# Optimization experiments

Measured on AMD Instinct MI355X. Metric: run time of the kernel, lower is better.

The kernel has to match this reference:

```python
import jax, jax.numpy as jnp
import numpy as np

B, S, D, H = 2, 2048, 1024, 16
HD = D // H  # head_dim = 64


def setup_inputs() -> dict:
    key = jax.random.key(0)
    ks = jax.random.split(key, 7)
    s = 0.02
    return {
        "queries": jax.random.normal(ks[0], (B, S, D), jnp.float32),
        "keys": jax.random.normal(ks[1], (B, S, D), jnp.float32),
        "values": jax.random.normal(ks[2], (B, S, D), jnp.float32),
        "Wq": jax.random.normal(ks[3], (D, D), jnp.float32) * s,
        "Wk": jax.random.normal(ks[4], (D, D), jnp.float32) * s,
        "Wv": jax.random.normal(ks[5], (D, D), jnp.float32) * s,
        "Wo": jax.random.normal(ks[6], (D, D), jnp.float32) * s,
    }


def reference(queries, keys, values, Wq, Wk, Wv, Wo):
    # Projections (torch Linear: x @ W.T); split into heads -> [B, H, S, HD]
    def split_heads(x):
        b, s, _ = x.shape
        return x.reshape(b, s, H, HD).transpose(0, 2, 1, 3)

    q = split_heads(queries @ Wq.T)
    k = split_heads(keys @ Wk.T)
    v = split_heads(values @ Wv.T)

    scale = 1.0 / jnp.sqrt(jnp.asarray(HD, q.dtype))
    scores = jnp.einsum("bhqd,bhkd->bhqk", q, k) * scale  # [B,H,S,S]
    attn = jax.nn.softmax(scores, axis=-1)
    ctx = jnp.einsum("bhqk,bhkd->bhqd", attn, v)  # [B,H,S,HD]
    out = ctx.transpose(0, 2, 1, 3).reshape(queries.shape[0], -1, D)
    return out @ Wo.T
```

## Files before the change

### kernel.cpp

```cpp
#include <hip/hip_runtime.h>
#include <hip/hip_bf16.h>
#include <cstdint>


#define B_ 2
#define S_ 2048
#define D_ 1024
#define H_ 16
#define HD_ 64
#define NE_ (B_ * S_ * D_)
#define WN_ (D_ * D_)

typedef unsigned short u16;
typedef unsigned int u32;
typedef u16 __attribute__((may_alias)) u16_ma;
typedef float __attribute__((may_alias)) f32_ma;
typedef u32 v4u __attribute__((ext_vector_type(4)));
typedef v4u __attribute__((may_alias)) v4u_ma;
typedef short bf16x8 __attribute__((ext_vector_type(8)));
typedef bf16x8 __attribute__((may_alias)) bf16x8_ma;
typedef float f32x4 __attribute__((ext_vector_type(4)));

__device__ __forceinline__ float bf2f(u16 u) {
  u32 x = ((u32)u) << 16;
  return __builtin_bit_cast(float, x);
}
__device__ __forceinline__ u16 f2bf(float f) {
  __hip_bfloat16 h = __float2bfloat16(f);
  return __builtin_bit_cast(u16, h);
}
__device__ __forceinline__ u32 pk2(u32 alo, u32 ahi) {
  return (u32)f2bf(__builtin_bit_cast(float, alo)) |
         ((u32)f2bf(__builtin_bit_cast(float, ahi)) << 16);
}

__device__ __forceinline__ void gl_lds16(const u16* g, u16* l) {
  auto gp = (const __attribute__((address_space(1))) unsigned int*)(const void*)g;
  auto lp = (__attribute__((address_space(3))) unsigned int*)(void*)l;
  __builtin_amdgcn_global_load_lds(gp, lp, 16, 0, 0);
}

__device__ __forceinline__ bool detect_f32(const u16* Wg) {
  const int lane = threadIdx.x & 63;
  bool hit = false;
#pragma unroll
  for (int i = 0; i < 4; ++i) {
    v4u u = *(const v4u_ma*)(Wg + lane * 32 + i * 8);
#pragma unroll
    for (int j = 0; j < 4; ++j) {
      u32 w = u[j];
      hit |= (((w >> 7) & 0xFFu) >= 0xF0u) || (((w >> 23) & 0xFFu) >= 0xF0u);
    }
  }
  return __any(hit);
}

__global__ __launch_bounds__(256) void convert_bf16(
    const void* s0, const void* s1, const void* s2, const void* s3,
    const void* s4, const void* s5, const void* s6, u16* __restrict__ dst_in,
    u16* __restrict__ dst_w, const u16* __restrict__ Wdet) {
  const bool det = detect_f32(Wdet);
  const int y = blockIdx.y;
  const void* src;
  u16* dst;
  int n;
  if (y < 3) {
    src = (y == 0) ? s0 : ((y == 1) ? s1 : s2);
    dst = dst_in + (size_t)y * NE_;
    n = NE_;
  } else {
    src = (y == 3) ? s3 : ((y == 4) ? s4 : ((y == 5) ? s5 : s6));
    dst = dst_w + (size_t)(y - 3) * WN_;
    n = WN_;
  }
  const int i = (blockIdx.x * 256 + threadIdx.x) * 8;
  if (i >= n) return;
  v4u out;
  if (det) {
    const v4u_ma* fp = (const v4u_ma*)((const float*)src + i);
    v4u f0 = fp[0], f1 = fp[1];
    out[0] = pk2(f0[0], f0[1]);
    out[1] = pk2(f0[2], f0[3]);
    out[2] = pk2(f1[0], f1[1]);
    out[3] = pk2(f1[2], f1[3]);
  } else {
    out = *(const v4u_ma*)((const u16*)src + i);
  }
  *(v4u_ma*)(dst + i) = out;
}

template <int BN, bool OUT_DET>
__global__ __launch_bounds__(256) void proj_g(
    const u16* __restrict__ Ab, const u16* __restrict__ Wb,
    void* __restrict__ Cb, const u16* __restrict__ Wdet) {
  __shared__ u16 Al[128 * 32];
  __shared__ u16 Wl[BN * 32];

  const bool outf32 = OUT_DET ? detect_f32(Wdet) : false;

  const int tid = threadIdx.x;
  const int lane = tid & 63, wid = tid >> 6;
  const int lg = lane >> 4, li = lane & 15;
  const int wr = wid >> 1, wc = wid & 1;
  const int z = blockIdx.z;
  const u16* Ag = Ab + (size_t)z * NE_;
  const u16* Wg = Wb + (size_t)z * WN_;
  const int m0 = blockIdx.x * 128, n0 = blockIdx.y * BN;

  const int srow = wid * 16 + (lane >> 2);
  const int scol = (lane & 3) * 8;
  const u16* Asrc = Ag + (size_t)(m0 + srow) * D_ + scol;
  const u16* Wsrc = Wg + (size_t)(n0 + srow) * D_ + scol;
  u16* Adst = Al + (wid * 16) * 32;
  u16* Wdst = Wl + (wid * 16) * 32;

  constexpr int NF = BN / 32;
  f32x4 acc[4][NF];
#pragma unroll
  for (int m = 0; m < 4; ++m)
#pragma unroll
    for (int n = 0; n < NF; ++n) acc[m][n] = (f32x4){0.f, 0.f, 0.f, 0.f};

  for (int kt = 0; kt < 32; ++kt) {
    const int k0 = kt * 32;
    __syncthreads();
    gl_lds16(Asrc + k0, Adst);
    gl_lds16(Asrc + (size_t)64 * D_ + k0, Adst + 64 * 32);
    gl_lds16(Wsrc + k0, Wdst);
    if constexpr (BN == 128) gl_lds16(Wsrc + (size_t)64 * D_ + k0, Wdst + 64 * 32);
    __syncthreads();

    bf16x8 af[4], bw[NF];
#pragma unroll
    for (int m = 0; m < 4; ++m)
      af[m] = *(const bf16x8_ma*)(Al + (wr * 64 + m * 16 + li) * 32 + lg * 8);
#pragma unroll
    for (int n = 0; n < NF; ++n)
      bw[n] =
          *(const bf16x8_ma*)(Wl + (wc * (BN / 2) + n * 16 + li) * 32 + lg * 8);
#pragma unroll
    for (int m = 0; m < 4; ++m)
#pragma unroll
      for (int n = 0; n < NF; ++n)
        acc[m][n] =
            __builtin_amdgcn_mfma_f32_16x16x32_bf16(af[m], bw[n], acc[m][n], 0, 0, 0);
  }

#pragma unroll
  for (int m = 0; m < 4; ++m)
#pragma unroll
    for (int n = 0; n < NF; ++n)
#pragma unroll
      for (int r = 0; r < 4; ++r) {
        const int row = m0 + wr * 64 + m * 16 + lg * 4 + r;
        const int col = n0 + wc * (BN / 2) + n * 16 + li;
        const size_t idx = (size_t)row * D_ + col;
        const float v = acc[m][n][r];
        if (OUT_DET) {
          if (outf32)
            ((f32_ma*)Cb)[idx] = v;
          else
            ((u16_ma*)Cb)[idx] = f2bf(v);
        } else {
          ((u16_ma*)((u16*)Cb + (size_t)z * NE_))[idx] = f2bf(v);
        }
      }
}

__global__ __launch_bounds__(256) void attn_mfma2(
    const u16* __restrict__ Qg, const u16* __restrict__ Kg,
    const u16* __restrict__ Vg, u16* __restrict__ Og) {
  __shared__ u16 Kl[64 * 64];
  __shared__ u16 VTl[64 * 64];
  __shared__ u16 Pl[4][32 * 64];

  const int tid = threadIdx.x;
  const int wid = tid >> 6, lane = tid & 63;
  const int lg = lane >> 4, li = lane & 15;

  const int bid = blockIdx.x;
  const int swz = (bid & 7) * 64 + (bid >> 3);
  const int qb = swz & 15;
  const int h = (swz >> 4) & 15;
  const int b = swz >> 8;
  const size_t bbase = (size_t)b * S_ * D_;
  const int hoff = h * HD_;
  const int q0 = qb * 128 + wid * 32;

  bf16x8 aq[2][2];
#pragma unroll
  for (int qf = 0; qf < 2; ++qf) {
    const u16* qp =
        Qg + bbase + (size_t)(q0 + qf * 16 + li) * D_ + hoff + lg * 8;
    aq[qf][0] = *(const bf16x8_ma*)(qp);
    aq[qf][1] = *(const bf16x8_ma*)(qp + 32);
  }

  f32x4 o[2][4];
  float mrun[2][4], lrun[2][4];
#pragma unroll
  for (int qf = 0; qf < 2; ++qf)
#pragma unroll
    for (int t = 0; t < 4; ++t) {
      o[qf][t] = (f32x4){0.f, 0.f, 0.f, 0.f};
      mrun[qf][t] = -1e30f;
      lrun[qf][t] = 0.f;
    }

  const int krr = tid >> 3;
  const int kc8 = (tid & 7) * 8;
  const int vkr = lane;
  const int vd0 = wid * 8;

  v4u kr0, kr1, vr0, vr1;
  auto kv_load = [&](int kt) {
    const int key0 = kt * 64;
    kr0 = *(const v4u_ma*)(Kg + bbase + (size_t)(key0 + krr) * D_ + hoff + kc8);
    kr1 = *(const v4u_ma*)(Kg + bbase + (size_t)(key0 + 32 + krr) * D_ + hoff + kc8);
    vr0 = *(const v4u_ma*)(Vg + bbase + (size_t)(key0 + vkr) * D_ + hoff + vd0);
    vr1 = *(const v4u_ma*)(Vg + bbase + (size_t)(key0 + vkr) * D_ + hoff + vd0 + 32);
  };
  auto kv_write = [&]() {
    const int ksw = (krr & 7) << 4;
    *(v4u_ma*)((char*)Kl + krr * 128 + ((kc8 * 2) ^ ksw)) = kr0;
    *(v4u_ma*)((char*)Kl + (32 + krr) * 128 + ((kc8 * 2) ^ ksw)) = kr1;
    union {
      v4u v;
      u16 e[8];
    } uu;
    uu.v = vr0;
#pragma unroll
    for (int j = 0; j < 8; ++j) {
      const int d = vd0 + j;
      *(u16*)((char*)VTl + d * 128 + ((vkr * 2) ^ ((d & 7) << 4))) = uu.e[j];
    }
    uu.v = vr1;
#pragma unroll
    for (int j = 0; j < 8; ++j) {
      const int d = vd0 + 32 + j;
      *(u16*)((char*)VTl + d * 128 + ((vkr * 2) ^ ((d & 7) << 4))) = uu.e[j];
    }
  };

  kv_load(0);
  kv_write();

  for (int kt = 0; kt < S_ / 64; ++kt) {
    __syncthreads();
    if (kt < S_ / 64 - 1) kv_load(kt + 1);

    f32x4 s[2][4];
#pragma unroll
    for (int kk = 0; kk < 4; ++kk) {
      const int row = kk * 16 + li;
      const char* kb = (const char*)Kl + row * 128;
      const int sw = (row & 7) << 4;
      bf16x8 b0 = *(const bf16x8_ma*)(kb + ((lg * 16) ^ sw));
      bf16x8 b1 = *(const bf16x8_ma*)(kb + ((64 + lg * 16) ^ sw));
#pragma unroll
      for (int qf = 0; qf < 2; ++qf) {
        f32x4 z = (f32x4){0.f, 0.f, 0.f, 0.f};
        z = __builtin_amdgcn_mfma_f32_16x16x32_bf16(aq[qf][0], b0, z, 0, 0, 0);
        z = __builtin_amdgcn_mfma_f32_16x16x32_bf16(aq[qf][1], b1, z, 0, 0, 0);
        s[qf][kk] = z * 0.125f;
      }
    }

#pragma unroll
    for (int qf = 0; qf < 2; ++qf) {
      float al[4];
#pragma unroll
      for (int r = 0; r < 4; ++r) {
        float t0 =
            fmaxf(fmaxf(s[qf][0][r], s[qf][1][r]), fmaxf(s[qf][2][r], s[qf][3][r]));
#pragma unroll
        for (int off = 1; off < 16; off <<= 1) t0 = fmaxf(t0, __shfl_xor(t0, off));
        const float mn = fmaxf(mrun[qf][r], t0);
        al[r] = __expf(mrun[qf][r] - mn);
        mrun[qf][r] = mn;
      }
#pragma unroll
      for (int r = 0; r < 4; ++r) {
        s[qf][0][r] = __expf(s[qf][0][r] - mrun[qf][r]);
        s[qf][1][r] = __expf(s[qf][1][r] - mrun[qf][r]);
        s[qf][2][r] = __expf(s[qf][2][r] - mrun[qf][r]);
        s[qf][3][r] = __expf(s[qf][3][r] - mrun[qf][r]);
        float sum = s[qf][0][r] + s[qf][1][r] + s[qf][2][r] + s[qf][3][r];
#pragma unroll
        for (int off = 1; off < 16; off <<= 1) sum += __shfl_xor(sum, off);
        lrun[qf][r] = lrun[qf][r] * al[r] + sum;
      }
      const f32x4 alv = {al[0], al[1], al[2], al[3]};
#pragma unroll
      for (int t = 0; t < 4; ++t) o[qf][t] *= alv;
    }

    char* Pw = (char*)&Pl[wid][0];
#pragma unroll
    for (int qf = 0; qf < 2; ++qf)
#pragma unroll
      for (int kk = 0; kk < 4; ++kk)
#pragma unroll
        for (int r = 0; r < 4; ++r) {
          const int row = qf * 16 + lg * 4 + r;
          *(u16*)(Pw + row * 128 + (((kk * 16 + li) * 2) ^ ((row & 7) << 4))) =
              f2bf(s[qf][kk][r]);
        }
    asm volatile("s_waitcnt lgkmcnt(0)" ::: "memory");

    bf16x8 pa[2][2];
#pragma unroll
    for (int qf = 0; qf < 2; ++qf) {
      const char* pb = Pw + (qf * 16 + li) * 128;
      const int sw = (li & 7) << 4;
      pa[qf][0] = *(const bf16x8_ma*)(pb + ((lg * 16) ^ sw));
      pa[qf][1] = *(const bf16x8_ma*)(pb + ((64 + lg * 16) ^ sw));
    }

#pragma unroll
    for (int t = 0; t < 4; ++t) {
      const int row = t * 16 + li;
      const char* vb = (const char*)VTl + row * 128;
      const int sw = (row & 7) << 4;
      bf16x8 v0 = *(const bf16x8_ma*)(vb + ((lg * 16) ^ sw));
      bf16x8 v1 = *(const bf16x8_ma*)(vb + ((64 + lg * 16) ^ sw));
#pragma unroll
      for (int qf = 0; qf < 2; ++qf) {
        o[qf][t] =
            __builtin_amdgcn_mfma_f32_16x16x32_bf16(pa[qf][0], v0, o[qf][t], 0, 0, 0);
        o[qf][t] =
            __builtin_amdgcn_mfma_f32_16x16x32_bf16(pa[qf][1], v1, o[qf][t], 0, 0, 0);
      }
    }

    __syncthreads();
    if (kt < S_ / 64 - 1) kv_write();
  }

#pragma unroll
  for (int qf = 0; qf < 2; ++qf)
#pragma unroll
    for (int r = 0; r < 4; ++r) {
      const float inv = 1.f / lrun[qf][r];
      const int q = q0 + qf * 16 + lg * 4 + r;
      u16* op = Og + bbase + (size_t)q * D_ + hoff + li;
#pragma unroll
      for (int t = 0; t < 4; ++t) op[t * 16] = f2bf(o[qf][t][r] * inv);
    }
}

template <bool A_SCR, bool SCR_F32, bool OUT_FINAL>
__global__ __launch_bounds__(256) void proj_slow(
    const void* __restrict__ Ag, const u16* __restrict__ Wg,
    void* __restrict__ Cg) {
  const bool det = detect_f32(Wg);
  const bool a_f32 = A_SCR ? SCR_F32 : det;
  const int m = blockIdx.x;
  const int n = blockIdx.y * 256 + threadIdx.x;
  const size_t arow = (size_t)m * D_;
  const size_t wrow = (size_t)n * D_;
  float acc = 0.f;
  for (int k = 0; k < D_; ++k) {
    float a = a_f32 ? ((const f32_ma*)Ag)[arow + k]
                    : bf2f(((const u16_ma*)Ag)[arow + k]);
    float w = det ? ((const f32_ma*)Wg)[wrow + k]
                  : bf2f(((const u16_ma*)Wg)[wrow + k]);
    acc += a * w;
  }
  const size_t ci = (size_t)m * D_ + n;
  const bool c_f32 = OUT_FINAL ? det : SCR_F32;
  if (c_f32)
    ((f32_ma*)Cg)[ci] = acc;
  else
    ((u16_ma*)Cg)[ci] = f2bf(acc);
}

template <bool SCR_F32>
__global__ __launch_bounds__(256) void attn_slow(
    const void* __restrict__ Qg, const void* __restrict__ Kg,
    const void* __restrict__ Vg, void* __restrict__ Cg) {
  const int tid = threadIdx.x;
  const int qblk = blockIdx.x & 7;
  const int h = (blockIdx.x >> 3) & 15;
  const int b = blockIdx.x >> 7;
  const int q = qblk * 256 + tid;
  const size_t base = (size_t)b * S_ * D_;
  const int hoff = h * HD_;
  float qv[64];
  {
    const size_t qrow = base + (size_t)q * D_ + hoff;
    for (int d = 0; d < 64; ++d)
      qv[d] = SCR_F32 ? ((const f32_ma*)Qg)[qrow + d]
                      : bf2f(((const u16_ma*)Qg)[qrow + d]);
  }
  float o[64];
  for (int d = 0; d < 64; ++d) o[d] = 0.f;
  float m = -1e30f, l = 0.f;
  for (int key = 0; key < S_; ++key) {
    const size_t krow = base + (size_t)key * D_ + hoff;
    float s = 0.f;
    for (int d = 0; d < 64; ++d) {
      float kx = SCR_F32 ? ((const f32_ma*)Kg)[krow + d]
                         : bf2f(((const u16_ma*)Kg)[krow + d]);
      s += qv[d] * kx;
    }
    s *= 0.125f;
    float mn = fmaxf(m, s);
    float al = expf(m - mn);
    float pe = expf(s - mn);
    m = mn;
    l = l * al + pe;
    for (int d = 0; d < 64; ++d) {
      float vx = SCR_F32 ? ((const f32_ma*)Vg)[krow + d]
                         : bf2f(((const u16_ma*)Vg)[krow + d]);
      o[d] = o[d] * al + pe * vx;
    }
  }
  const float il = 1.f / l;
  const size_t crow = base + (size_t)q * D_ + hoff;
  for (int d = 0; d < 64; ++d) {
    if (SCR_F32)
      ((f32_ma*)Cg)[crow + d] = o[d] * il;
    else
      ((u16_ma*)Cg)[crow + d] = f2bf(o[d] * il);
  }
}

extern "C" void kernel_launch(void* const* d_in, const int* in_sizes, int n_in,
                              void* d_out, int out_size, void* d_ws,
                              size_t ws_size, hipStream_t stream) {
  const u16* Wdet = (const u16*)d_in[3];
  dim3 blk(256);

  if (ws_size >= (size_t)4 * NE_ * sizeof(float)) {
    u16* Qi = (u16*)d_ws;
    u16* Wc = Qi + (size_t)3 * NE_;
    u16* Qp = Wc + (size_t)4 * WN_;
    u16* Xp = Qp + (size_t)3 * NE_;

    convert_bf16<<<dim3(2048, 7), blk, 0, stream>>>(
        d_in[0], d_in[1], d_in[2], d_in[3], d_in[4], d_in[5], d_in[6], Qi, Wc,
        Wdet);
    proj_g<128, false><<<dim3(32, 8, 3), blk, 0, stream>>>(Qi, Wc, Qp, Wdet);
    attn_mfma2<<<dim3(512), blk, 0, stream>>>(Qp, Qp + NE_, Qp + (size_t)2 * NE_,
                                              Xp);
    proj_g<64, true><<<dim3(32, 16, 1), blk, 0, stream>>>(
        Xp, Wc + (size_t)3 * WN_, d_out, Wdet);
  } else {
    dim3 gproj(B_ * S_, D_ / 256);
    dim3 gattn(B_ * H_ * (S_ / 256));
    u16* Qp = (u16*)d_out;
    u16* Kp = (u16*)d_in[0];
    u16* Vp = (u16*)d_in[1];
    u16* Xp = (u16*)d_in[2];
    proj_slow<false, false, false><<<gproj, blk, 0, stream>>>(
        d_in[0], (const u16*)d_in[3], Qp);
    proj_slow<false, false, false><<<gproj, blk, 0, stream>>>(
        d_in[1], (const u16*)d_in[4], Kp);
    proj_slow<false, false, false><<<gproj, blk, 0, stream>>>(
        d_in[2], (const u16*)d_in[5], Vp);
    attn_slow<false><<<gattn, blk, 0, stream>>>(Qp, Kp, Vp, Xp);
    proj_slow<true, false, true><<<gproj, blk, 0, stream>>>(
        Xp, (const u16*)d_in[6], d_out);
  }
}
```

Baseline: 283.9 us.

## Rewrite attention with 32x32 MFMA transposed scores and register-resident P; widen GEMM K-tile

The attention kernel now computes transposed scores S^T with 32x32x16 MFMAs, so each lane owns one query row. Softmax P is then repacked in registers with cross-half shuffles instead of a round trip through LDS, and the output rescale is skipped unless the running max grows by more than 8. The projection GEMM loads 64-wide K tiles with an XOR-swizzled LDS layout and folds the 1/sqrt(d) scale into the Q projection output. The goals are fewer LDS round trips and barriers and higher MFMA throughput per step; the cost is more register pressure and a lazy-rescale numerical tolerance.

```diff
diff --git a/kernel.cpp b/kernel.cpp
--- a/kernel.cpp
+++ b/kernel.cpp
@@ -1,6 +1,5 @@
 #include <hip/hip_runtime.h>
 #include <hip/hip_bf16.h>
-#include <cstdint>
 
 
 #define B_ 2
@@ -20,6 +19,7 @@
 typedef short bf16x8 __attribute__((ext_vector_type(8)));
 typedef bf16x8 __attribute__((may_alias)) bf16x8_ma;
 typedef float f32x4 __attribute__((ext_vector_type(4)));
+typedef float f32x16 __attribute__((ext_vector_type(16)));
 
 __device__ __forceinline__ float bf2f(u16 u) {
   u32 x = ((u32)u) << 16;
@@ -32,6 +32,9 @@
 __device__ __forceinline__ u32 pk2(u32 alo, u32 ahi) {
   return (u32)f2bf(__builtin_bit_cast(float, alo)) |
          ((u32)f2bf(__builtin_bit_cast(float, ahi)) << 16);
+}
+__device__ __forceinline__ u32 pkf(float lo, float hi) {
+  return (u32)f2bf(lo) | ((u32)f2bf(hi) << 16);
 }
 
 __device__ __forceinline__ void gl_lds16(const u16* g, u16* l) {
@@ -93,8 +96,8 @@
 __global__ __launch_bounds__(256) void proj_g(
     const u16* __restrict__ Ab, const u16* __restrict__ Wb,
     void* __restrict__ Cb, const u16* __restrict__ Wdet) {
-  __shared__ u16 Al[128 * 32];
-  __shared__ u16 Wl[BN * 32];
+  __shared__ u16 Al[128 * 64];
+  __shared__ u16 Wl[BN * 64];
 
   const bool outf32 = OUT_DET ? detect_f32(Wdet) : false;
 
@@ -103,16 +106,12 @@
   const int lg = lane >> 4, li = lane & 15;
   const int wr = wid >> 1, wc = wid & 1;
   const int z = blockIdx.z;
-  const u16* Ag = Ab + (size_t)z * NE_;
-  const u16* Wg = Wb + (size_t)z * WN_;
+  const char* Ag = (const char*)(Ab + (size_t)z * NE_);
+  const char* Wg = (const char*)(Wb + (size_t)z * WN_);
   const int m0 = blockIdx.x * 128, n0 = blockIdx.y * BN;
 
-  const int srow = wid * 16 + (lane >> 2);
-  const int scol = (lane & 3) * 8;
-  const u16* Asrc = Ag + (size_t)(m0 + srow) * D_ + scol;
-  const u16* Wsrc = Wg + (size_t)(n0 + srow) * D_ + scol;
-  u16* Adst = Al + (wid * 16) * 32;
-  u16* Wdst = Wl + (wid * 16) * 32;
+  const int lr = lane >> 3;
+  const int swzb = ((lane & 7) * 16) ^ (lr << 4);
 
   constexpr int NF = BN / 32;
   f32x4 acc[4][NF];
@@ -121,31 +120,57 @@
 #pragma unroll
     for (int n = 0; n < NF; ++n) acc[m][n] = (f32x4){0.f, 0.f, 0.f, 0.f};
 
-  for (int kt = 0; kt < 32; ++kt) {
-    const int k0 = kt * 32;
+  for (int kt = 0; kt < 16; ++kt) {
+    const int k0b = kt * 128;
     __syncthreads();
-    gl_lds16(Asrc + k0, Adst);
-    gl_lds16(Asrc + (size_t)64 * D_ + k0, Adst + 64 * 32);
-    gl_lds16(Wsrc + k0, Wdst);
-    if constexpr (BN == 128) gl_lds16(Wsrc + (size_t)64 * D_ + k0, Wdst + 64 * 32);
+#pragma unroll
+    for (int c = 0; c < 4; ++c) {
+      const int row = wid * 32 + c * 8 + lr;
+      gl_lds16((const u16*)(Ag + (size_t)(m0 + row) * 2048 + k0b + swzb),
+               Al + (wid * 32 + c * 8) * 64);
+    }
+    if constexpr (BN == 128) {
+#pragma unroll
+      for (int c = 0; c < 4; ++c) {
+        const int row = wid * 32 + c * 8 + lr;
+        gl_lds16((const u16*)(Wg + (size_t)(n0 + row) * 2048 + k0b + swzb),
+                 Wl + (wid * 32 + c * 8) * 64);
+      }
+    } else {
+#pragma unroll
+      for (int c = 0; c < 2; ++c) {
+        const int row = wid * 16 + c * 8 + lr;
+        gl_lds16((const u16*)(Wg + (size_t)(n0 + row) * 2048 + k0b + swzb),
+                 Wl + (wid * 16 + c * 8) * 64);
+      }
+    }
     __syncthreads();
 
-    bf16x8 af[4], bw[NF];
-#pragma unroll
-    for (int m = 0; m < 4; ++m)
-      af[m] = *(const bf16x8_ma*)(Al + (wr * 64 + m * 16 + li) * 32 + lg * 8);
-#pragma unroll
-    for (int n = 0; n < NF; ++n)
-      bw[n] =
-          *(const bf16x8_ma*)(Wl + (wc * (BN / 2) + n * 16 + li) * 32 + lg * 8);
-#pragma unroll
-    for (int m = 0; m < 4; ++m)
-#pragma unroll
-      for (int n = 0; n < NF; ++n)
-        acc[m][n] =
-            __builtin_amdgcn_mfma_f32_16x16x32_bf16(af[m], bw[n], acc[m][n], 0, 0, 0);
-  }
-
+#pragma unroll
+    for (int ks = 0; ks < 2; ++ks) {
+      bf16x8 af[4], bw[NF];
+#pragma unroll
+      for (int m = 0; m < 4; ++m) {
+        const int row = wr * 64 + m * 16 + li;
+        af[m] = *(const bf16x8_ma*)((const char*)Al + row * 128 +
+                                    ((ks * 64 + lg * 16) ^ ((row & 7) << 4)));
+      }
+#pragma unroll
+      for (int n = 0; n < NF; ++n) {
+        const int row = wc * (BN / 2) + n * 16 + li;
+        bw[n] = *(const bf16x8_ma*)((const char*)Wl + row * 128 +
+                                    ((ks * 64 + lg * 16) ^ ((row & 7) << 4)));
+      }
+#pragma unroll
+      for (int m = 0; m < 4; ++m)
+#pragma unroll
+        for (int n = 0; n < NF; ++n)
+          acc[m][n] = __builtin_amdgcn_mfma_f32_16x16x32_bf16(af[m], bw[n],
+                                                              acc[m][n], 0, 0, 0);
+    }
+  }
+
+  const float zs = (!OUT_DET && z == 0) ? 0.125f : 1.0f;
 #pragma unroll
   for (int m = 0; m < 4; ++m)
 #pragma unroll
@@ -155,7 +180,7 @@
         const int row = m0 + wr * 64 + m * 16 + lg * 4 + r;
         const int col = n0 + wc * (BN / 2) + n * 16 + li;
         const size_t idx = (size_t)row * D_ + col;
-        const float v = acc[m][n][r];
+        const float v = acc[m][n][r] * zs;
         if (OUT_DET) {
           if (outf32)
             ((f32_ma*)Cb)[idx] = v;
@@ -167,16 +192,16 @@
       }
 }
 
-__global__ __launch_bounds__(256) void attn_mfma2(
+__global__ __launch_bounds__(256) void attn3(
     const u16* __restrict__ Qg, const u16* __restrict__ Kg,
     const u16* __restrict__ Vg, u16* __restrict__ Og) {
   __shared__ u16 Kl[64 * 64];
   __shared__ u16 VTl[64 * 64];
-  __shared__ u16 Pl[4][32 * 64];
 
   const int tid = threadIdx.x;
   const int wid = tid >> 6, lane = tid & 63;
-  const int lg = lane >> 4, li = lane & 15;
+  const int l31 = lane & 31;
+  const int hi = lane >> 5;
 
   const int bid = blockIdx.x;
   const int swz = (bid & 7) * 64 + (bid >> 3);
@@ -185,27 +210,23 @@
   const int b = swz >> 8;
   const size_t bbase = (size_t)b * S_ * D_;
   const int hoff = h * HD_;
-  const int q0 = qb * 128 + wid * 32;
-
-  bf16x8 aq[2][2];
-#pragma unroll
-  for (int qf = 0; qf < 2; ++qf) {
-    const u16* qp =
-        Qg + bbase + (size_t)(q0 + qf * 16 + li) * D_ + hoff + lg * 8;
-    aq[qf][0] = *(const bf16x8_ma*)(qp);
-    aq[qf][1] = *(const bf16x8_ma*)(qp + 32);
-  }
-
-  f32x4 o[2][4];
-  float mrun[2][4], lrun[2][4];
-#pragma unroll
-  for (int qf = 0; qf < 2; ++qf)
-#pragma unroll
-    for (int t = 0; t < 4; ++t) {
-      o[qf][t] = (f32x4){0.f, 0.f, 0.f, 0.f};
-      mrun[qf][t] = -1e30f;
-      lrun[qf][t] = 0.f;
-    }
+  const int q0w = qb * 128 + wid * 32;
+
+  bf16x8 bq[4];
+  {
+    const u16* qp = Qg + bbase + (size_t)(q0w + l31) * D_ + hoff + hi * 8;
+#pragma unroll
+    for (int dblk = 0; dblk < 4; ++dblk)
+      bq[dblk] = *(const bf16x8_ma*)(qp + dblk * 16);
+  }
+
+  f32x16 o0, o1;
+#pragma unroll
+  for (int i = 0; i < 16; ++i) {
+    o0[i] = 0.f;
+    o1[i] = 0.f;
+  }
+  float mrun = -1e30f, lrun = 0.f;
 
   const int krr = tid >> 3;
   const int kc8 = (tid & 7) * 8;
@@ -245,108 +266,107 @@
   kv_load(0);
   kv_write();
 
+  const int swk = (l31 & 7) << 4;
+
   for (int kt = 0; kt < S_ / 64; ++kt) {
     __syncthreads();
     if (kt < S_ / 64 - 1) kv_load(kt + 1);
 
-    f32x4 s[2][4];
-#pragma unroll
-    for (int kk = 0; kk < 4; ++kk) {
-      const int row = kk * 16 + li;
-      const char* kb = (const char*)Kl + row * 128;
-      const int sw = (row & 7) << 4;
-      bf16x8 b0 = *(const bf16x8_ma*)(kb + ((lg * 16) ^ sw));
-      bf16x8 b1 = *(const bf16x8_ma*)(kb + ((64 + lg * 16) ^ sw));
-#pragma unroll
-      for (int qf = 0; qf < 2; ++qf) {
-        f32x4 z = (f32x4){0.f, 0.f, 0.f, 0.f};
-        z = __builtin_amdgcn_mfma_f32_16x16x32_bf16(aq[qf][0], b0, z, 0, 0, 0);
-        z = __builtin_amdgcn_mfma_f32_16x16x32_bf16(aq[qf][1], b1, z, 0, 0, 0);
-        s[qf][kk] = z * 0.125f;
-      }
-    }
-
-#pragma unroll
-    for (int qf = 0; qf < 2; ++qf) {
-      float al[4];
-#pragma unroll
-      for (int r = 0; r < 4; ++r) {
-        float t0 =
-            fmaxf(fmaxf(s[qf][0][r], s[qf][1][r]), fmaxf(s[qf][2][r], s[qf][3][r]));
-#pragma unroll
-        for (int off = 1; off < 16; off <<= 1) t0 = fmaxf(t0, __shfl_xor(t0, off));
-        const float mn = fmaxf(mrun[qf][r], t0);
-        al[r] = __expf(mrun[qf][r] - mn);
-        mrun[qf][r] = mn;
-      }
-#pragma unroll
-      for (int r = 0; r < 4; ++r) {
-        s[qf][0][r] = __expf(s[qf][0][r] - mrun[qf][r]);
-        s[qf][1][r] = __expf(s[qf][1][r] - mrun[qf][r]);
-        s[qf][2][r] = __expf(s[qf][2][r] - mrun[qf][r]);
-        s[qf][3][r] = __expf(s[qf][3][r] - mrun[qf][r]);
-        float sum = s[qf][0][r] + s[qf][1][r] + s[qf][2][r] + s[qf][3][r];
-#pragma unroll
-        for (int off = 1; off < 16; off <<= 1) sum += __shfl_xor(sum, off);
-        lrun[qf][r] = lrun[qf][r] * al[r] + sum;
-      }
-      const f32x4 alv = {al[0], al[1], al[2], al[3]};
-#pragma unroll
-      for (int t = 0; t < 4; ++t) o[qf][t] *= alv;
-    }
-
-    char* Pw = (char*)&Pl[wid][0];
-#pragma unroll
-    for (int qf = 0; qf < 2; ++qf)
-#pragma unroll
-      for (int kk = 0; kk < 4; ++kk)
-#pragma unroll
-        for (int r = 0; r < 4; ++r) {
-          const int row = qf * 16 + lg * 4 + r;
-          *(u16*)(Pw + row * 128 + (((kk * 16 + li) * 2) ^ ((row & 7) << 4))) =
-              f2bf(s[qf][kk][r]);
+    f32x16 sT0, sT1;
+#pragma unroll
+    for (int i = 0; i < 16; ++i) {
+      sT0[i] = 0.f;
+      sT1[i] = 0.f;
+    }
+    __builtin_amdgcn_s_setprio(1);
+#pragma unroll
+    for (int dblk = 0; dblk < 4; ++dblk) {
+      const int cb = (dblk * 32 + hi * 16);
+      bf16x8 a0 = *(const bf16x8_ma*)((const char*)Kl + l31 * 128 + (cb ^ swk));
+      bf16x8 a1 =
+          *(const bf16x8_ma*)((const char*)Kl + (32 + l31) * 128 + (cb ^ swk));
+      sT0 = __builtin_amdgcn_mfma_f32_32x32x16_bf16(a0, bq[dblk], sT0, 0, 0, 0);
+      sT1 = __builtin_amdgcn_mfma_f32_32x32x16_bf16(a1, bq[dblk], sT1, 0, 0, 0);
+    }
+    __builtin_amdgcn_s_setprio(0);
+
+    float pmax = sT0[0];
+#pragma unroll
+    for (int i = 1; i < 16; ++i) pmax = fmaxf(pmax, sT0[i]);
+#pragma unroll
+    for (int i = 0; i < 16; ++i) pmax = fmaxf(pmax, sT1[i]);
+    pmax = fmaxf(pmax, __shfl_xor(pmax, 32));
+    if (!__all(pmax - mrun <= 8.f)) {
+      const float mnew = fmaxf(mrun, pmax);
+      const float al = __expf(mrun - mnew);
+      mrun = mnew;
+      lrun *= al;
+      o0 *= al;
+      o1 *= al;
+    }
+
+    u32 w[16];
+    float sum = 0.f;
+#pragma unroll
+    for (int kh = 0; kh < 2; ++kh)
+#pragma unroll
+      for (int g = 0; g < 4; ++g)
+#pragma unroll
+        for (int u = 0; u < 2; ++u) {
+          const int r = g * 4 + 2 * u;
+          const float pe =
+              __expf((kh ? sT1[r] : sT0[r]) - mrun);
+          const float po =
+              __expf((kh ? sT1[r + 1] : sT0[r + 1]) - mrun);
+          sum += pe + po;
+          w[kh * 8 + g * 2 + u] = pkf(pe, po);
         }
-    asm volatile("s_waitcnt lgkmcnt(0)" ::: "memory");
-
-    bf16x8 pa[2][2];
-#pragma unroll
-    for (int qf = 0; qf < 2; ++qf) {
-      const char* pb = Pw + (qf * 16 + li) * 128;
-      const int sw = (li & 7) << 4;
-      pa[qf][0] = *(const bf16x8_ma*)(pb + ((lg * 16) ^ sw));
-      pa[qf][1] = *(const bf16x8_ma*)(pb + ((64 + lg * 16) ^ sw));
-    }
-
-#pragma unroll
-    for (int t = 0; t < 4; ++t) {
-      const int row = t * 16 + li;
-      const char* vb = (const char*)VTl + row * 128;
-      const int sw = (row & 7) << 4;
-      bf16x8 v0 = *(const bf16x8_ma*)(vb + ((lg * 16) ^ sw));
-      bf16x8 v1 = *(const bf16x8_ma*)(vb + ((64 + lg * 16) ^ sw));
-#pragma unroll
-      for (int qf = 0; qf < 2; ++qf) {
-        o[qf][t] =
-            __builtin_amdgcn_mfma_f32_16x16x32_bf16(pa[qf][0], v0, o[qf][t], 0, 0, 0);
-        o[qf][t] =
-            __builtin_amdgcn_mfma_f32_16x16x32_bf16(pa[qf][1], v1, o[qf][t], 0, 0, 0);
-      }
-    }
+    sum += __shfl_xor(sum, 32);
+    lrun += sum;
+
+    bf16x8 pf[4];
+#pragma unroll
+    for (int km = 0; km < 4; ++km) {
+      const int a = 4 * km;
+      const u32 s0 = hi ? w[a] : w[a + 2];
+      const u32 s1 = hi ? w[a + 1] : w[a + 3];
+      const u32 r0 = (u32)__shfl_xor((int)s0, 32);
+      const u32 r1 = (u32)__shfl_xor((int)s1, 32);
+      union {
+        u32 d[4];
+        bf16x8 v;
+      } uu;
+      uu.d[0] = hi ? r0 : w[a];
+      uu.d[1] = hi ? r1 : w[a + 1];
+      uu.d[2] = hi ? w[a + 2] : r0;
+      uu.d[3] = hi ? w[a + 3] : r1;
+      pf[km] = uu.v;
+    }
+
+    __builtin_amdgcn_s_setprio(1);
+#pragma unroll
+    for (int km = 0; km < 4; ++km) {
+      const int cb = (km * 32 + hi * 16);
+      bf16x8 v0 = *(const bf16x8_ma*)((const char*)VTl + l31 * 128 + (cb ^ swk));
+      bf16x8 v1 =
+          *(const bf16x8_ma*)((const char*)VTl + (32 + l31) * 128 + (cb ^ swk));
+      o0 = __builtin_amdgcn_mfma_f32_32x32x16_bf16(v0, pf[km], o0, 0, 0, 0);
+      o1 = __builtin_amdgcn_mfma_f32_32x32x16_bf16(v1, pf[km], o1, 0, 0, 0);
+    }
+    __builtin_amdgcn_s_setprio(0);
 
     __syncthreads();
     if (kt < S_ / 64 - 1) kv_write();
   }
 
-#pragma unroll
-  for (int qf = 0; qf < 2; ++qf)
-#pragma unroll
-    for (int r = 0; r < 4; ++r) {
-      const float inv = 1.f / lrun[qf][r];
-      const int q = q0 + qf * 16 + lg * 4 + r;
-      u16* op = Og + bbase + (size_t)q * D_ + hoff + li;
-#pragma unroll
-      for (int t = 0; t < 4; ++t) op[t * 16] = f2bf(o[qf][t][r] * inv);
-    }
+  const float inv = 1.f / lrun;
+  u16* orow = Og + bbase + (size_t)(q0w + l31) * D_ + hoff;
+#pragma unroll
+  for (int r = 0; r < 16; ++r) {
+    const int d0 = (r & 3) + 8 * (r >> 2) + 4 * hi;
+    orow[d0] = f2bf(o0[r] * inv);
+    orow[d0 + 32] = f2bf(o1[r] * inv);
+  }
 }
 
 template <bool A_SCR, bool SCR_F32, bool OUT_FINAL>
@@ -442,8 +462,7 @@
         d_in[0], d_in[1], d_in[2], d_in[3], d_in[4], d_in[5], d_in[6], Qi, Wc,
         Wdet);
     proj_g<128, false><<<dim3(32, 8, 3), blk, 0, stream>>>(Qi, Wc, Qp, Wdet);
-    attn_mfma2<<<dim3(512), blk, 0, stream>>>(Qp, Qp + NE_, Qp + (size_t)2 * NE_,
-                                              Xp);
+    attn3<<<dim3(512), blk, 0, stream>>>(Qp, Qp + NE_, Qp + (size_t)2 * NE_, Xp);
     proj_g<64, true><<<dim3(32, 16, 1), blk, 0, stream>>>(
         Xp, Wc + (size_t)3 * WN_, d_out, Wdet);
   } else {
```

After: 228.9 us. 19.4% less time.
